# Kernel optimization log

Measured on AMD Instinct MI355X. Metric: run time of the kernel, lower is better.

Reference implementation:

```python
import jax, jax.numpy as jnp
import numpy as np

B, C, N, V, W = 2, 4, 224, 7, 256
EMB, H = 256, 4
TOKEN_DIM = C * N           # 896
HF = int(C * 2.66)          # 10 (GDFN hidden features)
EPS_LN = 1e-6


def _dwconv3(x, w):
    # depthwise 3x3, padding=1; x:[B,Ch,Hh,Ww], w:[Ch,1,3,3]
    return jax.lax.conv_general_dilated(
        x, w, window_strides=(1, 1), padding='SAME',
        feature_group_count=x.shape[1],
        dimension_numbers=('NCHW', 'OIHW', 'NCHW'))


def _layernorm_c(x, g, b):
    # LayerNorm over channel dim (NCHW), eps=1e-6
    m = jnp.mean(x, axis=1, keepdims=True)
    v = jnp.mean((x - m) ** 2, axis=1, keepdims=True)
    return (x - m) / jnp.sqrt(v + EPS_LN) * g[None, :, None, None] + b[None, :, None, None]


def setup_inputs() -> dict:
    key = jax.random.key(0)
    ks = jax.random.split(key, 12)
    s = 0.02
    return {
        'buffer':     jax.random.normal(ks[0], (B, C, N, V, W), jnp.float32),
        'w_in':       jax.random.normal(ks[1], (EMB, TOKEN_DIM), jnp.float32) * s,
        'temperature': jnp.ones((1, H, 1, 1), jnp.float32),
        'ln1_g':      jnp.ones((EMB,), jnp.float32),
        'ln1_b':      jnp.zeros((EMB,), jnp.float32),
        'w_qkv':      jax.random.normal(ks[2], (3 * EMB, EMB), jnp.float32) * s,
        'w_qkv_dw':   jax.random.normal(ks[3], (3 * EMB, 1, 3, 3), jnp.float32) * s,
        'w_proj':     jax.random.normal(ks[4], (TOKEN_DIM, EMB), jnp.float32) * s,
        'w_attca':    jax.random.normal(ks[5], (2 * H, H), jnp.float32) * s,
        'ln2_g':      jnp.ones((C,), jnp.float32),
        'ln2_b':      jnp.zeros((C,), jnp.float32),
        'w_pin':      jax.random.normal(ks[6], (2 * HF, C), jnp.float32) * s,
        'w_dw':       jax.random.normal(ks[7], (2 * HF, 1, 3, 3), jnp.float32) * s,
        'w_pout':     jax.random.normal(ks[8], (C, HF), jnp.float32) * s,
    }


def reference(buffer, w_in, temperature, ln1_g, ln1_b, w_qkv, w_qkv_dw,
              w_proj, w_attca, ln2_g, ln2_b, w_pin, w_dw, w_pout):
    S = V * W
    d = EMB // H
    # b c n v w -> b (v w) (c n)
    x_tok = buffer.transpose(0, 3, 4, 1, 2).reshape(B, S, C * N)
    # b c n v w -> (b n) c v w
    x_res = buffer.transpose(0, 2, 1, 3, 4).reshape(B * N, C, V, W)

    x_tok = jnp.einsum('bsk,ek->bse', x_tok, w_in)                  # linear_in
    x = x_tok.reshape(B, V, W, EMB).transpose(0, 3, 1, 2)           # b emb v w
    x_norm = _layernorm_c(x, ln1_g, ln1_b)

    qkv = jnp.einsum('bchw,oc->bohw', x_norm, w_qkv)                # 1x1 conv
    qkv = _dwconv3(qkv, w_qkv_dw)
    q, k, v_ = jnp.split(qkv, 3, axis=1)

    def heads(t):  # b (h d) v w -> b h (v w) d
        return t.reshape(B, H, d, S).transpose(0, 1, 3, 2)
    q, k, v_ = heads(q), heads(k), heads(v_)

    # F.normalize(dim=-1), eps=1e-12
    q = q / jnp.maximum(jnp.linalg.norm(q, axis=-1, keepdims=True), 1e-12)
    k = k / jnp.maximum(jnp.linalg.norm(k, axis=-1, keepdims=True), 1e-12)

    attn_logits = jnp.einsum('bhid,bhjd->bhij', q, k) * temperature
    attn0 = jax.nn.softmax(attn_logits, axis=-1)
    attn1 = jnp.maximum(attn_logits, 0.0) ** 2
    attn1 = jax.nn.gelu(attn1, approximate=False) * attn1
    x_att = jnp.einsum('bhij,oh->boij', attn1, w_attca)             # 1x1 conv over heads
    scale, shift = jnp.split(x_att, 2, axis=1)
    attn = attn0 * (1.0 + scale) + shift

    out = jnp.einsum('bhij,bhjd->bhid', attn, v_)
    out = out.transpose(0, 1, 3, 2).reshape(B, EMB, V, W)           # b (h d) v w
    out = jnp.einsum('bchw,oc->bohw', out, w_proj)                  # proj to token_dim
    out = out.reshape(B, C, N, V, W).transpose(0, 2, 1, 3, 4).reshape(B * N, C, V, W)

    x2 = x_res + out
    epi = _layernorm_c(x2, ln2_g, ln2_b)
    # GDFN
    h_ = jnp.einsum('bchw,oc->bohw', epi, w_pin)
    h_ = _dwconv3(h_, w_dw)
    h1, h2 = jnp.split(h_, 2, axis=1)
    h_ = jax.nn.gelu(h1, approximate=False) * h2
    epi = jnp.einsum('bchw,oc->bohw', h_, w_pout)
    epi = x2 + epi

    return epi.reshape(B, N, C, V, W).transpose(0, 2, 1, 3, 4)      # b c n v w
```

## Files before the change

kernel.cpp:

```cpp
#include <hip/hip_runtime.h>
#include <math.h>

#define B_ 2
#define C_ 4
#define N_ 224
#define V_ 7
#define W_ 256
#define S_ 1792
#define EMB_ 256
#define H_ 4
#define D_ 64
#define TOK_ 896
#define HF_ 10
#define JC_ 8
#define JRANGE_ (S_ / JC_)
#define JSTEPS_ (JRANGE_ / 32)

typedef __attribute__((ext_vector_type(8))) short short8;
typedef __attribute__((ext_vector_type(4))) float f32x4;

#define MFMA16(a, b, c) __builtin_amdgcn_mfma_f32_16x16x32_bf16(a, b, c, 0, 0, 0)

__device__ inline short f2bf(float f) {
    union { float f; unsigned u; } x; x.f = f;
    unsigned u = x.u;
    unsigned r = (u + 0x7fffu + ((u >> 16) & 1u)) >> 16;
    return (short)r;
}
__device__ inline float bf2f(short s) {
    union { unsigned u; float f; } x;
    x.u = ((unsigned)(unsigned short)s) << 16;
    return x.f;
}
__device__ inline unsigned cvtpk_bf16(float lo, float hi) {
    unsigned r;
    asm("v_cvt_pk_bf16_f32 %0, %1, %2" : "=v"(r) : "v"(lo), "v"(hi));
    return r;
}

template<bool COLSUM, bool LNB, bool BBF>
__global__ __launch_bounds__(256) void gemm_kernel(
    const float* __restrict__ A, const void* __restrict__ Bv, float* __restrict__ Cm,
    int M, int N, int K, long b_bs, long c_bs,
    const float* __restrict__ csin, float* __restrict__ csout,
    const float* __restrict__ lg, const float* __restrict__ lb)
{
    const int bz = blockIdx.z;
    Cm += (long)bz * c_bs;
    const int m0 = blockIdx.y * 64, n0 = blockIdx.x * 128;
    __shared__ __align__(16) short As[64 * 32];
    __shared__ __align__(16) short Bs[128 * 32];
    const int t = threadIdx.x;
    const int lane = t & 63, wave = t >> 6;
    const int wr = wave >> 1, wc = wave & 1;
    const int col = lane & 15, grp = lane >> 4;
    const int arow = t >> 2, akc = (t & 3) * 8;
    const int bn = t & 127, bkc = (t >> 7) * 16;
    float mean = 0.f, rstd = 1.f;
    if (LNB) {
        float s = 0.f, q = 0.f;
        #pragma unroll
        for (int mb = 0; mb < 4; ++mb) {
            s += csin[((long)(bz * 4 + mb) * 2 + 0) * N + n0 + bn];
            q += csin[((long)(bz * 4 + mb) * 2 + 1) * N + n0 + bn];
        }
        mean = s * (1.f / 256.f);
        rstd = rsqrtf(q * (1.f / 256.f) - mean * mean + 1e-6f);
    }
    f32x4 acc[2][4];
    #pragma unroll
    for (int i = 0; i < 2; ++i)
        #pragma unroll
        for (int j = 0; j < 4; ++j) acc[i][j] = (f32x4){0.f, 0.f, 0.f, 0.f};
    for (int k0 = 0; k0 < K; k0 += 32) {
        {
            const float* ap = &A[(long)(m0 + arow) * K + k0 + akc];
            f32x4 a0 = *(const f32x4*)ap;
            f32x4 a1 = *(const f32x4*)(ap + 4);
            short8 av;
            av[0] = f2bf(a0[0]); av[1] = f2bf(a0[1]); av[2] = f2bf(a0[2]); av[3] = f2bf(a0[3]);
            av[4] = f2bf(a1[0]); av[5] = f2bf(a1[1]); av[6] = f2bf(a1[2]); av[7] = f2bf(a1[3]);
            int abyte = (arow << 6) + (akc << 1);
            *(short8*)((char*)As + (abyte ^ ((arow & 7) << 4))) = av;
        }
        {
            short8 b0, b1;
            if (BBF) {
                const short* Bp = (const short*)Bv + (long)bz * b_bs;
                #pragma unroll
                for (int j = 0; j < 8; ++j) {
                    b0[j] = Bp[(long)(k0 + bkc + j) * N + n0 + bn];
                    b1[j] = Bp[(long)(k0 + bkc + 8 + j) * N + n0 + bn];
                }
            } else {
                const float* Bp = (const float*)Bv + (long)bz * b_bs;
                #pragma unroll
                for (int j = 0; j < 16; ++j) {
                    float v = Bp[(long)(k0 + bkc + j) * N + n0 + bn];
                    if (LNB) v = fmaf((v - mean) * rstd, lg[k0 + bkc + j], lb[k0 + bkc + j]);
                    if (j < 8) b0[j] = f2bf(v); else b1[j - 8] = f2bf(v);
                }
            }
            int bbyte = (bn << 6) + (bkc << 1);
            *(short8*)((char*)Bs + ((bbyte) ^ ((bn & 7) << 4))) = b0;
            *(short8*)((char*)Bs + ((bbyte + 16) ^ ((bn & 7) << 4))) = b1;
        }
        __syncthreads();
        short8 af[2], bfv[4];
        #pragma unroll
        for (int mm = 0; mm < 2; ++mm) {
            int r = wr * 32 + mm * 16 + col;
            af[mm] = *(const short8*)((const char*)As + (((r << 6) + (grp << 4)) ^ ((r & 7) << 4)));
        }
        #pragma unroll
        for (int nn = 0; nn < 4; ++nn) {
            int r = wc * 64 + nn * 16 + col;
            bfv[nn] = *(const short8*)((const char*)Bs + (((r << 6) + (grp << 4)) ^ ((r & 7) << 4)));
        }
        #pragma unroll
        for (int mm = 0; mm < 2; ++mm)
            #pragma unroll
            for (int nn = 0; nn < 4; ++nn)
                acc[mm][nn] = MFMA16(af[mm], bfv[nn], acc[mm][nn]);
        __syncthreads();
    }
    #pragma unroll
    for (int mm = 0; mm < 2; ++mm)
        #pragma unroll
        for (int nn = 0; nn < 4; ++nn)
            #pragma unroll
            for (int r = 0; r < 4; ++r)
                Cm[(long)(m0 + wr * 32 + mm * 16 + grp * 4 + r) * N
                   + n0 + wc * 64 + nn * 16 + col] = acc[mm][nn][r];
    if (COLSUM) {
        float* red = (float*)As;
        #pragma unroll
        for (int nn = 0; nn < 4; ++nn) {
            float s = 0.f, q = 0.f;
            #pragma unroll
            for (int mm = 0; mm < 2; ++mm)
                #pragma unroll
                for (int r = 0; r < 4; ++r) { float v = acc[mm][nn][r]; s += v; q += v * v; }
            s += __shfl_xor(s, 16, 64); s += __shfl_xor(s, 32, 64);
            q += __shfl_xor(q, 16, 64); q += __shfl_xor(q, 32, 64);
            if (lane < 16) {
                int cidx = wc * 64 + nn * 16 + col;
                red[(wr * 128 + cidx) * 2]     = s;
                red[(wr * 128 + cidx) * 2 + 1] = q;
            }
        }
        __syncthreads();
        if (wave < 2 && lane < 16) {
            #pragma unroll
            for (int nn = 0; nn < 4; ++nn) {
                int cidx = wc * 64 + nn * 16 + col;
                float s = red[cidx * 2]     + red[(128 + cidx) * 2];
                float q = red[cidx * 2 + 1] + red[(128 + cidx) * 2 + 1];
                csout[((long)(bz * 4 + blockIdx.y) * 2 + 0) * N + n0 + cidx] = s;
                csout[((long)(bz * 4 + blockIdx.y) * 2 + 1) * N + n0 + cidx] = q;
            }
        }
    }
}

__global__ void dwconv3_kernel(const float* __restrict__ X, const float* __restrict__ Wt,
                               float* __restrict__ Y, short* __restrict__ vbf,
                               long total, int Ch)
{
    long idx = (long)blockIdx.x * blockDim.x + threadIdx.x;
    long stride = (long)gridDim.x * blockDim.x;
    for (; idx < total; idx += stride) {
        int w = (int)(idx % W_);
        long t = idx / W_;
        int h = (int)(t % V_); t /= V_;
        int ch = (int)(t % Ch);
        long img_ch = idx / ((long)V_ * W_);
        const float* wp = Wt + ch * 9;
        const float* xp = X + img_ch * (V_ * W_);
        float acc = 0.f;
        #pragma unroll
        for (int dy = -1; dy <= 1; ++dy) {
            int h2 = h + dy;
            if (h2 < 0 || h2 >= V_) continue;
            #pragma unroll
            for (int dx = -1; dx <= 1; ++dx) {
                int w2 = w + dx;
                if (w2 < 0 || w2 >= W_) continue;
                acc += xp[h2 * W_ + w2] * wp[(dy + 1) * 3 + (dx + 1)];
            }
        }
        Y[idx] = acc;
        if (vbf && ch >= 512) {
            int b = (int)(t / Ch);
            vbf[((long)b * 256 + (ch - 512)) * S_ + h * W_ + w] = f2bf(acc);
        }
    }
}

__global__ __launch_bounds__(256) void headnorm_kernel(
    const float* __restrict__ qkvd, const float* __restrict__ temp,
    short* __restrict__ qn, short* __restrict__ kn)
{
    int s0 = blockIdx.x * 64;
    int bh = blockIdx.y; int b = bh >> 2, h = bh & 3;
    int isq = blockIdx.z;
    int ch0 = b * 768 + (isq ? 0 : EMB_) + h * 64;
    short* dst = (isq ? qn : kn) + (long)bh * S_ * 64;
    __shared__ float tile[64][65];
    __shared__ float red[64][4];
    int t = threadIdx.x;
    int sl = t & 63, dg = t >> 6;
    float part = 0.f;
    for (int dd = 0; dd < 16; ++dd) {
        int d = dg * 16 + dd;
        float v = qkvd[(long)(ch0 + d) * S_ + s0 + sl];
        tile[sl][d] = v;
        part += v * v;
    }
    red[sl][dg] = part;
    __syncthreads();
    int d = t & 63, sg = t >> 6;
    float tmul = isq ? temp[h] : 1.f;
    for (int si = 0; si < 16; ++si) {
        int s = sg * 16 + si;
        float nrm = sqrtf(red[s][0] + red[s][1] + red[s][2] + red[s][3]);
        float scale = tmul / fmaxf(nrm, 1e-12f);
        dst[(long)(s0 + s) * 64 + d] = f2bf(tile[s][d] * scale);
    }
}

__global__ __launch_bounds__(256) void attn_kernel(
    const short* __restrict__ qn, const short* __restrict__ kn,
    const short* __restrict__ vbf, const float* __restrict__ wat,
    short* __restrict__ partY, float* __restrict__ partZ)
{
    const int h = threadIdx.x >> 6;
    const int lane = threadIdx.x & 63;
    const int col = lane & 15, grp = lane >> 4;
    const int itile = blockIdx.x;
    const int jc = blockIdx.y;
    const int b = blockIdx.z;
    const int ibase = itile * 16;
    const int bh = b * 4 + h;

    const short* qrow = qn + ((long)bh * S_ + ibase + col) * 64 + grp * 8;
    short8 qa0 = *(const short8*)qrow;
    short8 qa1 = *(const short8*)(qrow + 32);
    float wsc[4], wsh[4];
    #pragma unroll
    for (int hh = 0; hh < 4; ++hh) { wsc[hh] = wat[h * 4 + hh]; wsh[hh] = wat[(4 + h) * 4 + hh]; }

    __shared__ float exch[2][4][32][34];

    f32x4 y1[4], y2[4];
    #pragma unroll
    for (int dt = 0; dt < 4; ++dt) {
        y1[dt] = (f32x4){0.f, 0.f, 0.f, 0.f};
        y2[dt] = (f32x4){0.f, 0.f, 0.f, 0.f};
    }
    float z = 0.f;
    const short* kbase = kn + (long)bh * S_ * 64;
    const short* vbase = vbf + ((long)b * 256 + h * 64) * S_;
    const int joffA = (col & 3) + 8 * (col >> 2);
    const int jbase0 = jc * JRANGE_;

    short8 kc0, kc1, kc2, kc3, vc0, vc1, vc2, vc3;
    {
        const short* kr0 = kbase + (long)(jbase0 + joffA) * 64 + grp * 8;
        const short* kr1 = kbase + (long)(jbase0 + joffA + 4) * 64 + grp * 8;
        kc0 = *(const short8*)kr0; kc1 = *(const short8*)(kr0 + 32);
        kc2 = *(const short8*)kr1; kc3 = *(const short8*)(kr1 + 32);
        const short* vr = vbase + (long)col * S_ + jbase0 + grp * 8;
        vc0 = *(const short8*)vr;
        vc1 = *(const short8*)(vr + 16 * S_);
        vc2 = *(const short8*)(vr + 32 * S_);
        vc3 = *(const short8*)(vr + 48 * S_);
    }

    for (int jt = 0; jt < JSTEPS_; ++jt) {
        const int jbase = jbase0 + jt * 32;
        const int buf = jt & 1;
        short8 kp0, kp1, kp2, kp3, vp0, vp1, vp2, vp3;
        if (jt + 1 < JSTEPS_) {
            const int jb2 = jbase + 32;
            const short* kr0 = kbase + (long)(jb2 + joffA) * 64 + grp * 8;
            const short* kr1 = kbase + (long)(jb2 + joffA + 4) * 64 + grp * 8;
            kp0 = *(const short8*)kr0; kp1 = *(const short8*)(kr0 + 32);
            kp2 = *(const short8*)kr1; kp3 = *(const short8*)(kr1 + 32);
            const short* vr = vbase + (long)col * S_ + jb2 + grp * 8;
            vp0 = *(const short8*)vr;
            vp1 = *(const short8*)(vr + 16 * S_);
            vp2 = *(const short8*)(vr + 32 * S_);
            vp3 = *(const short8*)(vr + 48 * S_);
        } else {
            kp0 = kc0; kp1 = kc1; kp2 = kc2; kp3 = kc3;
            vp0 = vc0; vp1 = vc1; vp2 = vc2; vp3 = vc3;
        }
        f32x4 lf[2];
        {
            f32x4 a = (f32x4){0.f, 0.f, 0.f, 0.f};
            a = MFMA16(kc0, qa0, a);
            a = MFMA16(kc1, qa1, a);
            lf[0] = a;
        }
        {
            f32x4 a = (f32x4){0.f, 0.f, 0.f, 0.f};
            a = MFMA16(kc2, qa0, a);
            a = MFMA16(kc3, qa1, a);
            lf[1] = a;
        }
        float a1own[2][4], ee[2][4];
        #pragma unroll
        for (int tt = 0; tt < 2; ++tt)
            #pragma unroll
            for (int r = 0; r < 4; ++r) {
                float l = lf[tt][r];
                float rr = fmaxf(l, 0.f);
                float s1 = rr * rr;
                float u = fmaf(s1 * s1, 0.0713548162726f * s1, 1.59576912161f * s1);
                float sg = __builtin_amdgcn_rcpf(1.f + __expf(-u));
                float a1 = s1 * sg * s1;
                a1own[tt][r] = a1;
                ee[tt][r] = __expf(l);
                exch[buf][h][r + 4 * tt + 8 * grp][col] = a1;
            }
        __syncthreads();
        union { short8 s; unsigned u[4]; } pa_, pb_;
        #pragma unroll
        for (int tt = 0; tt < 2; ++tt) {
            float scv[4], shv[4];
            #pragma unroll
            for (int r = 0; r < 4; ++r) {
                int jloc = r + 4 * tt + 8 * grp;
                float sc = 0.f, sh = 0.f;
                #pragma unroll
                for (int hh = 0; hh < 4; ++hh) {
                    float a1v = (hh == h) ? a1own[tt][r] : exch[buf][hh][jloc][col];
                    sc += a1v * wsc[hh];
                    sh += a1v * wsh[hh];
                }
                float e = ee[tt][r];
                z += e;
                scv[r] = e * (1.f + sc);
                shv[r] = sh;
            }
            pa_.u[tt * 2]     = cvtpk_bf16(scv[0], scv[1]);
            pa_.u[tt * 2 + 1] = cvtpk_bf16(scv[2], scv[3]);
            pb_.u[tt * 2]     = cvtpk_bf16(shv[0], shv[1]);
            pb_.u[tt * 2 + 1] = cvtpk_bf16(shv[2], shv[3]);
        }
        y1[0] = MFMA16(pa_.s, vc0, y1[0]); y2[0] = MFMA16(pb_.s, vc0, y2[0]);
        y1[1] = MFMA16(pa_.s, vc1, y1[1]); y2[1] = MFMA16(pb_.s, vc1, y2[1]);
        y1[2] = MFMA16(pa_.s, vc2, y1[2]); y2[2] = MFMA16(pb_.s, vc2, y2[2]);
        y1[3] = MFMA16(pa_.s, vc3, y1[3]); y2[3] = MFMA16(pb_.s, vc3, y2[3]);
        kc0 = kp0; kc1 = kp1; kc2 = kp2; kc3 = kp3;
        vc0 = vp0; vc1 = vp1; vc2 = vp2; vc3 = vp3;
    }

    z += __shfl_xor(z, 16, 64);
    z += __shfl_xor(z, 32, 64);
    if (grp == 0)
        partZ[((long)(jc * 2 + b) * 4 + h) * S_ + ibase + col] = z;

    __syncthreads();
    float* tb = &exch[0][h][0][0];
    long ybase = ((((long)jc * 2 + b) * 4 + h) * 2) * 64 * S_;
    for (int acc = 0; acc < 2; ++acc) {
        #pragma unroll
        for (int dt = 0; dt < 4; ++dt) {
            f32x4 y = acc ? y2[dt] : y1[dt];
            #pragma unroll
            for (int r = 0; r < 4; ++r) tb[(grp * 4 + r) * 17 + col] = y[r];
            #pragma unroll
            for (int p = 0; p < 4; ++p) {
                float val = tb[col * 17 + p * 4 + grp];
                partY[ybase + ((long)acc * 64 + dt * 16 + p * 4 + grp) * S_ + ibase + col] = f2bf(val);
            }
        }
    }
}

__global__ __launch_bounds__(256) void combine_kernel(
    const short* __restrict__ partY, const float* __restrict__ partZ,
    short* __restrict__ outav)
{
    int idx = blockIdx.x * 256 + threadIdx.x;
    int i = idx % S_;
    int t = idx / S_;
    int d = t & 63; t >>= 6;
    int h = t & 3; int b = t >> 2;
    float y1 = 0.f, y2 = 0.f, z = 0.f;
    #pragma unroll
    for (int jc = 0; jc < JC_; ++jc) {
        long base = ((((long)jc * 2 + b) * 4 + h) * 2) * 64 * S_;
        y1 += bf2f(partY[base + (long)d * S_ + i]);
        y2 += bf2f(partY[base + (long)(64 + d) * S_ + i]);
        z  += partZ[((long)(jc * 2 + b) * 4 + h) * S_ + i];
    }
    outav[((long)b * 256 + h * 64 + d) * S_ + i] = f2bf(y1 / z + y2);
}

__global__ __launch_bounds__(256) void resid_pin_kernel(
    const float* __restrict__ buffer, const float* __restrict__ proj,
    const float* __restrict__ g2, const float* __restrict__ b2,
    const float* __restrict__ w_pin,
    float* __restrict__ x2, short* __restrict__ hbuf)
{
    int s = blockIdx.x * 256 + threadIdx.x;
    int bn = blockIdx.y;
    int b = bn / N_, n = bn % N_;
    float v[4];
    float sum = 0.f;
    #pragma unroll
    for (int c = 0; c < 4; ++c) {
        float xr = buffer[((long)(b * 4 + c) * N_ + n) * S_ + s];
        float pr = proj[((long)b * TOK_ + c * N_ + n) * S_ + s];
        v[c] = xr + pr;
        x2[((long)bn * 4 + c) * S_ + s] = v[c];
        sum += v[c];
    }
    float mean = sum * 0.25f;
    float var = 0.f;
    #pragma unroll
    for (int c = 0; c < 4; ++c) { float dd = v[c] - mean; var += dd * dd; }
    var *= 0.25f;
    float inv = rsqrtf(var + 1e-6f);
    float e[4];
    #pragma unroll
    for (int c = 0; c < 4; ++c) e[c] = (v[c] - mean) * inv * g2[c] + b2[c];
    for (int o = 0; o < 2 * HF_; ++o) {
        float a = 0.f;
        #pragma unroll
        for (int c = 0; c < 4; ++c) a += w_pin[o * 4 + c] * e[c];
        hbuf[((long)bn * (2 * HF_) + o) * S_ + s] = f2bf(a);
    }
}

__global__ __launch_bounds__(448) void gdfn_kernel(
    const short* __restrict__ hbuf, const float* __restrict__ w_dw,
    const float* __restrict__ w_pout, const float* __restrict__ x2,
    float* __restrict__ out)
{
    int xt = blockIdx.x;
    int bn = blockIdx.y;
    int b = bn / N_, n = bn % N_;
    int x0 = xt * 64;
    __shared__ float tile[20][7][66];
    int tid = threadIdx.x;
    for (int idx = tid; idx < 20 * 7 * 66; idx += 448) {
        int ch = idx / (7 * 66); int rem = idx % (7 * 66);
        int y = rem / 66; int xx = rem % 66;
        int gx = x0 + xx - 1;
        float v = 0.f;
        if (gx >= 0 && gx < W_) v = bf2f(hbuf[((long)bn * 20 + ch) * S_ + y * W_ + gx]);
        tile[ch][y][xx] = v;
    }
    __syncthreads();
    int y = tid / 64, x = tid & 63;
    float hd[20];
    #pragma unroll
    for (int ch = 0; ch < 20; ++ch) {
        const float* wp = w_dw + ch * 9;
        float acc = 0.f;
        #pragma unroll
        for (int dy = -1; dy <= 1; ++dy) {
            int yy = y + dy;
            if (yy < 0 || yy >= V_) continue;
            #pragma unroll
            for (int dx = -1; dx <= 1; ++dx)
                acc += tile[ch][yy][x + 1 + dx] * wp[(dy + 1) * 3 + (dx + 1)];
        }
        hd[ch] = acc;
    }
    float g[HF_];
    #pragma unroll
    for (int f = 0; f < HF_; ++f) {
        float h1 = hd[f];
        g[f] = 0.5f * h1 * (1.f + erff(h1 * 0.70710678118654752f)) * hd[HF_ + f];
    }
    int s = y * W_ + x0 + x;
    #pragma unroll
    for (int c = 0; c < 4; ++c) {
        float a = 0.f;
        #pragma unroll
        for (int f = 0; f < HF_; ++f) a += w_pout[c * HF_ + f] * g[f];
        out[((long)(b * 4 + c) * N_ + n) * S_ + s] = x2[((long)bn * 4 + c) * S_ + s] + a;
    }
}

extern "C" void kernel_launch(void* const* d_in, const int* in_sizes, int n_in,
                              void* d_out, int out_size, void* d_ws, size_t ws_size,
                              hipStream_t stream)
{
    const float* buffer = (const float*)d_in[0];
    const float* w_in   = (const float*)d_in[1];
    const float* temp   = (const float*)d_in[2];
    const float* ln1_g  = (const float*)d_in[3];
    const float* ln1_b  = (const float*)d_in[4];
    const float* w_qkv  = (const float*)d_in[5];
    const float* w_qkv_dw = (const float*)d_in[6];
    const float* w_proj = (const float*)d_in[7];
    const float* w_attca = (const float*)d_in[8];
    const float* ln2_g  = (const float*)d_in[9];
    const float* ln2_b  = (const float*)d_in[10];
    const float* w_pin  = (const float*)d_in[11];
    const float* w_dw   = (const float*)d_in[12];
    const float* w_pout = (const float*)d_in[13];
    float* out = (float*)d_out;

    float* ws = (float*)d_ws;
    float* qkvd    = ws;
    short* qn      = (short*)(ws + 2752512);
    short* kn      = (short*)(ws + 3211264);
    short* vbf     = (short*)(ws + 3670016);
    short* partY   = (short*)(ws + 4128768);
    float* partZ   = ws + 11468800;
    short* outav   = (short*)(ws + 11583488);
    float* xw      = ws + 12042240;
    float* colsum  = ws + 12959744;
    float* qkv     = ws + 12988416;
    float* outproj = ws + 15740928;
    float* x2      = ws + 18952192;
    short* hbuf    = (short*)(ws + 22163456);

    gemm_kernel<true, false, false><<<dim3(14, 4, 2), 256, 0, stream>>>(
        w_in, buffer, xw, EMB_, S_, TOK_, (long)TOK_ * S_, (long)EMB_ * S_,
        nullptr, colsum, nullptr, nullptr);

    gemm_kernel<false, true, false><<<dim3(14, 12, 2), 256, 0, stream>>>(
        w_qkv, xw, qkv, 3 * EMB_, S_, EMB_, (long)EMB_ * S_, (long)3 * EMB_ * S_,
        colsum, nullptr, ln1_g, ln1_b);

    {
        long total = (long)B_ * 3 * EMB_ * S_;
        dwconv3_kernel<<<(int)((total + 255) / 256), 256, 0, stream>>>(
            qkv, w_qkv_dw, qkvd, vbf, total, 3 * EMB_);
    }

    headnorm_kernel<<<dim3(28, 8, 2), 256, 0, stream>>>(qkvd, temp, qn, kn);

    attn_kernel<<<dim3(112, JC_, B_), 256, 0, stream>>>(qn, kn, vbf, w_attca, partY, partZ);

    combine_kernel<<<3584, 256, 0, stream>>>(partY, partZ, outav);

    gemm_kernel<false, false, true><<<dim3(14, 14, 2), 256, 0, stream>>>(
        w_proj, outav, outproj, TOK_, S_, EMB_, (long)EMB_ * S_, (long)TOK_ * S_,
        nullptr, nullptr, nullptr, nullptr);

    resid_pin_kernel<<<dim3(7, B_ * N_), 256, 0, stream>>>(
        buffer, outproj, ln2_g, ln2_b, w_pin, x2, hbuf);

    gdfn_kernel<<<dim3(4, B_ * N_), 448, 0, stream>>>(hbuf, w_dw, w_pout, x2, out);
}
```

Baseline: 197.5 us.

## Process two 16-row query tiles per attention block to reuse K/V loads

Each attention block now handles 32 query rows (two 16-row MFMA tiles) instead of 16, so every loaded K and V fragment feeds twice the MFMA work. The grid shrinks from 112 to 56 blocks in x. This cuts global K/V traffic per query. It raises register use from the doubled accumulators and halves the block count, which may reduce occupancy and latency hiding.

```diff
diff --git a/kernel.cpp b/kernel.cpp
--- a/kernel.cpp
+++ b/kernel.cpp
@@ -240,25 +240,30 @@
     const int itile = blockIdx.x;
     const int jc = blockIdx.y;
     const int b = blockIdx.z;
-    const int ibase = itile * 16;
+    const int ibase = itile * 32;
     const int bh = b * 4 + h;
 
-    const short* qrow = qn + ((long)bh * S_ + ibase + col) * 64 + grp * 8;
-    short8 qa0 = *(const short8*)qrow;
-    short8 qa1 = *(const short8*)(qrow + 32);
+    const short* qrow0 = qn + ((long)bh * S_ + ibase + col) * 64 + grp * 8;
+    const short* qrow1 = qrow0 + 16 * 64;
+    short8 qa0 = *(const short8*)qrow0;
+    short8 qa1 = *(const short8*)(qrow0 + 32);
+    short8 qb0 = *(const short8*)qrow1;
+    short8 qb1 = *(const short8*)(qrow1 + 32);
     float wsc[4], wsh[4];
     #pragma unroll
     for (int hh = 0; hh < 4; ++hh) { wsc[hh] = wat[h * 4 + hh]; wsh[hh] = wat[(4 + h) * 4 + hh]; }
 
     __shared__ float exch[2][4][32][34];
 
-    f32x4 y1[4], y2[4];
-    #pragma unroll
-    for (int dt = 0; dt < 4; ++dt) {
-        y1[dt] = (f32x4){0.f, 0.f, 0.f, 0.f};
-        y2[dt] = (f32x4){0.f, 0.f, 0.f, 0.f};
-    }
-    float z = 0.f;
+    f32x4 y1[2][4], y2[2][4];
+    #pragma unroll
+    for (int it = 0; it < 2; ++it)
+        #pragma unroll
+        for (int dt = 0; dt < 4; ++dt) {
+            y1[it][dt] = (f32x4){0.f, 0.f, 0.f, 0.f};
+            y2[it][dt] = (f32x4){0.f, 0.f, 0.f, 0.f};
+        }
+    float z0 = 0.f, z1 = 0.f;
     const short* kbase = kn + (long)bh * S_ * 64;
     const short* vbase = vbf + ((long)b * 256 + h * 64) * S_;
     const int joffA = (col & 3) + 8 * (col >> 2);
@@ -296,85 +301,142 @@
             kp0 = kc0; kp1 = kc1; kp2 = kc2; kp3 = kc3;
             vp0 = vc0; vp1 = vc1; vp2 = vc2; vp3 = vc3;
         }
-        f32x4 lf[2];
+        f32x4 lfA[2], lfB[2];
         {
             f32x4 a = (f32x4){0.f, 0.f, 0.f, 0.f};
-            a = MFMA16(kc0, qa0, a);
-            a = MFMA16(kc1, qa1, a);
-            lf[0] = a;
+            a = MFMA16(kc0, qa0, a); a = MFMA16(kc1, qa1, a); lfA[0] = a;
         }
         {
             f32x4 a = (f32x4){0.f, 0.f, 0.f, 0.f};
-            a = MFMA16(kc2, qa0, a);
-            a = MFMA16(kc3, qa1, a);
-            lf[1] = a;
-        }
-        float a1own[2][4], ee[2][4];
+            a = MFMA16(kc2, qa0, a); a = MFMA16(kc3, qa1, a); lfA[1] = a;
+        }
+        {
+            f32x4 a = (f32x4){0.f, 0.f, 0.f, 0.f};
+            a = MFMA16(kc0, qb0, a); a = MFMA16(kc1, qb1, a); lfB[0] = a;
+        }
+        {
+            f32x4 a = (f32x4){0.f, 0.f, 0.f, 0.f};
+            a = MFMA16(kc2, qb0, a); a = MFMA16(kc3, qb1, a); lfB[1] = a;
+        }
+        float a1A[2][4], eeA[2][4], a1B[2][4], eeB[2][4];
         #pragma unroll
         for (int tt = 0; tt < 2; ++tt)
             #pragma unroll
             for (int r = 0; r < 4; ++r) {
-                float l = lf[tt][r];
-                float rr = fmaxf(l, 0.f);
-                float s1 = rr * rr;
-                float u = fmaf(s1 * s1, 0.0713548162726f * s1, 1.59576912161f * s1);
-                float sg = __builtin_amdgcn_rcpf(1.f + __expf(-u));
-                float a1 = s1 * sg * s1;
-                a1own[tt][r] = a1;
-                ee[tt][r] = __expf(l);
-                exch[buf][h][r + 4 * tt + 8 * grp][col] = a1;
+                {
+                    float l = lfA[tt][r];
+                    float rr = fmaxf(l, 0.f);
+                    float s1 = rr * rr;
+                    float u = fmaf(s1 * s1, 0.0713548162726f * s1, 1.59576912161f * s1);
+                    float sg = __builtin_amdgcn_rcpf(1.f + __expf(-u));
+                    float a1 = s1 * sg * s1;
+                    a1A[tt][r] = a1;
+                    eeA[tt][r] = __expf(l);
+                    exch[buf][h][r + 4 * tt + 8 * grp][col] = a1;
+                }
+                {
+                    float l = lfB[tt][r];
+                    float rr = fmaxf(l, 0.f);
+                    float s1 = rr * rr;
+                    float u = fmaf(s1 * s1, 0.0713548162726f * s1, 1.59576912161f * s1);
+                    float sg = __builtin_amdgcn_rcpf(1.f + __expf(-u));
+                    float a1 = s1 * sg * s1;
+                    a1B[tt][r] = a1;
+                    eeB[tt][r] = __expf(l);
+                    exch[buf][h][r + 4 * tt + 8 * grp][col + 16] = a1;
+                }
             }
         __syncthreads();
-        union { short8 s; unsigned u[4]; } pa_, pb_;
-        #pragma unroll
-        for (int tt = 0; tt < 2; ++tt) {
-            float scv[4], shv[4];
-            #pragma unroll
-            for (int r = 0; r < 4; ++r) {
-                int jloc = r + 4 * tt + 8 * grp;
-                float sc = 0.f, sh = 0.f;
+        {
+            union { short8 s; unsigned u[4]; } pa_, pb_;
+            #pragma unroll
+            for (int tt = 0; tt < 2; ++tt) {
+                float scv[4], shv[4];
                 #pragma unroll
-                for (int hh = 0; hh < 4; ++hh) {
-                    float a1v = (hh == h) ? a1own[tt][r] : exch[buf][hh][jloc][col];
-                    sc += a1v * wsc[hh];
-                    sh += a1v * wsh[hh];
+                for (int r = 0; r < 4; ++r) {
+                    int jloc = r + 4 * tt + 8 * grp;
+                    float sc = 0.f, sh = 0.f;
+                    #pragma unroll
+                    for (int hh = 0; hh < 4; ++hh) {
+                        float a1v = (hh == h) ? a1A[tt][r] : exch[buf][hh][jloc][col];
+                        sc += a1v * wsc[hh];
+                        sh += a1v * wsh[hh];
+                    }
+                    float e = eeA[tt][r];
+                    z0 += e;
+                    scv[r] = e * (1.f + sc);
+                    shv[r] = sh;
                 }
-                float e = ee[tt][r];
-                z += e;
-                scv[r] = e * (1.f + sc);
-                shv[r] = sh;
-            }
-            pa_.u[tt * 2]     = cvtpk_bf16(scv[0], scv[1]);
-            pa_.u[tt * 2 + 1] = cvtpk_bf16(scv[2], scv[3]);
-            pb_.u[tt * 2]     = cvtpk_bf16(shv[0], shv[1]);
-            pb_.u[tt * 2 + 1] = cvtpk_bf16(shv[2], shv[3]);
-        }
-        y1[0] = MFMA16(pa_.s, vc0, y1[0]); y2[0] = MFMA16(pb_.s, vc0, y2[0]);
-        y1[1] = MFMA16(pa_.s, vc1, y1[1]); y2[1] = MFMA16(pb_.s, vc1, y2[1]);
-        y1[2] = MFMA16(pa_.s, vc2, y1[2]); y2[2] = MFMA16(pb_.s, vc2, y2[2]);
-        y1[3] = MFMA16(pa_.s, vc3, y1[3]); y2[3] = MFMA16(pb_.s, vc3, y2[3]);
+                pa_.u[tt * 2]     = cvtpk_bf16(scv[0], scv[1]);
+                pa_.u[tt * 2 + 1] = cvtpk_bf16(scv[2], scv[3]);
+                pb_.u[tt * 2]     = cvtpk_bf16(shv[0], shv[1]);
+                pb_.u[tt * 2 + 1] = cvtpk_bf16(shv[2], shv[3]);
+            }
+            y1[0][0] = MFMA16(pa_.s, vc0, y1[0][0]); y2[0][0] = MFMA16(pb_.s, vc0, y2[0][0]);
+            y1[0][1] = MFMA16(pa_.s, vc1, y1[0][1]); y2[0][1] = MFMA16(pb_.s, vc1, y2[0][1]);
+            y1[0][2] = MFMA16(pa_.s, vc2, y1[0][2]); y2[0][2] = MFMA16(pb_.s, vc2, y2[0][2]);
+            y1[0][3] = MFMA16(pa_.s, vc3, y1[0][3]); y2[0][3] = MFMA16(pb_.s, vc3, y2[0][3]);
+        }
+        {
+            union { short8 s; unsigned u[4]; } pa_, pb_;
+            #pragma unroll
+            for (int tt = 0; tt < 2; ++tt) {
+                float scv[4], shv[4];
+                #pragma unroll
+                for (int r = 0; r < 4; ++r) {
+                    int jloc = r + 4 * tt + 8 * grp;
+                    float sc = 0.f, sh = 0.f;
+                    #pragma unroll
+                    for (int hh = 0; hh < 4; ++hh) {
+                        float a1v = (hh == h) ? a1B[tt][r] : exch[buf][hh][jloc][col + 16];
+                        sc += a1v * wsc[hh];
+                        sh += a1v * wsh[hh];
+                    }
+                    float e = eeB[tt][r];
+                    z1 += e;
+                    scv[r] = e * (1.f + sc);
+                    shv[r] = sh;
+                }
+                pa_.u[tt * 2]     = cvtpk_bf16(scv[0], scv[1]);
+                pa_.u[tt * 2 + 1] = cvtpk_bf16(scv[2], scv[3]);
+                pb_.u[tt * 2]     = cvtpk_bf16(shv[0], shv[1]);
+                pb_.u[tt * 2 + 1] = cvtpk_bf16(shv[2], shv[3]);
+            }
+            y1[1][0] = MFMA16(pa_.s, vc0, y1[1][0]); y2[1][0] = MFMA16(pb_.s, vc0, y2[1][0]);
+            y1[1][1] = MFMA16(pa_.s, vc1, y1[1][1]); y2[1][1] = MFMA16(pb_.s, vc1, y2[1][1]);
+            y1[1][2] = MFMA16(pa_.s, vc2, y1[1][2]); y2[1][2] = MFMA16(pb_.s, vc2, y2[1][2]);
+            y1[1][3] = MFMA16(pa_.s, vc3, y1[1][3]); y2[1][3] = MFMA16(pb_.s, vc3, y2[1][3]);
+        }
         kc0 = kp0; kc1 = kp1; kc2 = kp2; kc3 = kp3;
         vc0 = vp0; vc1 = vp1; vc2 = vp2; vc3 = vp3;
     }
 
-    z += __shfl_xor(z, 16, 64);
-    z += __shfl_xor(z, 32, 64);
-    if (grp == 0)
-        partZ[((long)(jc * 2 + b) * 4 + h) * S_ + ibase + col] = z;
+    z0 += __shfl_xor(z0, 16, 64);
+    z0 += __shfl_xor(z0, 32, 64);
+    z1 += __shfl_xor(z1, 16, 64);
+    z1 += __shfl_xor(z1, 32, 64);
+    if (grp == 0) {
+        partZ[((long)(jc * 2 + b) * 4 + h) * S_ + ibase + col] = z0;
+        partZ[((long)(jc * 2 + b) * 4 + h) * S_ + ibase + 16 + col] = z1;
+    }
 
     __syncthreads();
     float* tb = &exch[0][h][0][0];
     long ybase = ((((long)jc * 2 + b) * 4 + h) * 2) * 64 * S_;
-    for (int acc = 0; acc < 2; ++acc) {
-        #pragma unroll
-        for (int dt = 0; dt < 4; ++dt) {
-            f32x4 y = acc ? y2[dt] : y1[dt];
-            #pragma unroll
-            for (int r = 0; r < 4; ++r) tb[(grp * 4 + r) * 17 + col] = y[r];
-            #pragma unroll
-            for (int p = 0; p < 4; ++p) {
-                float val = tb[col * 17 + p * 4 + grp];
-                partY[ybase + ((long)acc * 64 + dt * 16 + p * 4 + grp) * S_ + ibase + col] = f2bf(val);
+    #pragma unroll
+    for (int it = 0; it < 2; ++it) {
+        for (int acc = 0; acc < 2; ++acc) {
+            #pragma unroll
+            for (int dt = 0; dt < 4; ++dt) {
+                f32x4 y = acc ? y2[it][dt] : y1[it][dt];
+                #pragma unroll
+                for (int r = 0; r < 4; ++r) tb[(grp * 4 + r) * 17 + col] = y[r];
+                #pragma unroll
+                for (int p = 0; p < 4; ++p) {
+                    float val = tb[col * 17 + p * 4 + grp];
+                    partY[ybase + ((long)acc * 64 + dt * 16 + p * 4 + grp) * S_
+                          + ibase + it * 16 + col] = f2bf(val);
+                }
             }
         }
     }
@@ -539,7 +601,7 @@
 
     headnorm_kernel<<<dim3(28, 8, 2), 256, 0, stream>>>(qkvd, temp, qn, kn);
 
-    attn_kernel<<<dim3(112, JC_, B_), 256, 0, stream>>>(qn, kn, vbf, w_attca, partY, partZ);
+    attn_kernel<<<dim3(56, JC_, B_), 256, 0, stream>>>(qn, kn, vbf, w_attca, partY, partZ);
 
     combine_kernel<<<3584, 256, 0, stream>>>(partY, partZ, outav);
 
```

After: 195.1 us. Within noise of the previous version (-1.2%).
